# Kernel tuning notes

Hardware: AMD Instinct MI355X
Metric: run time of the kernel (lower is better)

The kernel has to match this reference:

```python
import jax, jax.numpy as jnp
import numpy as np

N_ENT = 2000
GAT_EMB = 64
GAT_HID = 3
HIDDEN = 256
BATCH = 8
ALPHA = 0.2  # LeakyReLU negative slope
MASK_FILL = jnp.float32(9e-15)  # original fills masked-out logits with 9e-15 (NOT -inf)


def setup_inputs() -> dict:
    key = jax.random.key(0)
    k1, k2, k3, k4, k5, k6 = jax.random.split(key, 6)
    emb = jax.random.normal(k1, (N_ENT, GAT_EMB), dtype=jnp.float32)
    W = jax.random.normal(k2, (GAT_EMB, GAT_HID), dtype=jnp.float32) * 0.2
    a = jax.random.normal(k3, (2 * GAT_HID, 1), dtype=jnp.float32) * 0.2
    fc1_w = jax.random.normal(k4, (HIDDEN, N_ENT * GAT_HID), dtype=jnp.float32) * 0.02
    fc1_b = jax.random.normal(k5, (HIDDEN,), dtype=jnp.float32) * 0.02
    adj = jax.random.randint(k6, (BATCH, N_ENT, N_ENT), 0, 2, dtype=jnp.int32)
    return {"emb": emb, "W": W, "a": a, "fc1_w": fc1_w, "fc1_b": fc1_b, "adj": adj}


def reference(emb, W, a, fc1_w, fc1_b, adj):
    # h = emb @ W : [N, 3] -- shared across all graphs in the batch
    h = emb @ W
    # Pairwise logits: original concatenates [h_i, h_j] and dots with a;
    # equivalent to (h @ a1)_i + (h @ a2)_j via broadcasting (no O(N^2*2H) tensor).
    s1 = h @ a[:GAT_HID, 0]   # [N]
    s2 = h @ a[GAT_HID:, 0]   # [N]
    e = jax.nn.leaky_relu(s1[:, None] + s2[None, :], negative_slope=ALPHA)  # [N, N]
    # Mask by adjacency (fill 9e-15, matching original), softmax over neighbors (dim=1)
    masked = jnp.where(adj > 0, e[None, :, :], MASK_FILL)  # [B, N, N]
    att = jax.nn.softmax(masked, axis=2)
    # Weighted aggregation + ELU (concat=True head)
    h_prime = jnp.einsum('bij,jd->bid', att, h)  # [B, N, 3]
    x = jax.nn.elu(h_prime).reshape(att.shape[0], -1)  # [B, N*3]
    return x @ fc1_w.T + fc1_b  # [B, hidden]
```

## Files before the change

kernel.cpp:

```cpp
#include <hip/hip_runtime.h>
#include <cstddef>

#define N_ENT   2000
#define GAT_EMB 64
#define HIDDEN  256
#define BATCH   8
#define ALPHA   0.2f

typedef _Float16 half4 __attribute__((ext_vector_type(4)));

#define WS_HX_OFF      8192
#define WS_HY_OFF      12288
#define WS_HZ_OFF      16384
#define WS_S1_OFF      20480
#define WS_TABLE_BYTES 28672
#define WS_X_OFF       28672
#define WS_TIER2_BYTES 124672

__global__ __launch_bounds__(256) void k_init(const float* __restrict__ fc1_b,
                                              float* __restrict__ out) {
    int idx = blockIdx.x * 256 + threadIdx.x;
    out[idx] = fc1_b[idx & (HIDDEN - 1)];
}

__global__ __launch_bounds__(256) void k_prep(const float* __restrict__ emb,
                                              const float* __restrict__ W,
                                              const float* __restrict__ a,
                                              float* __restrict__ ws) {
    __shared__ float sW[GAT_EMB * 3];
    __shared__ float sa[6];
    int t = threadIdx.x;
    if (t < GAT_EMB * 3) sW[t] = W[t];
    if (t < 6)           sa[t] = a[t];
    __syncthreads();
    int i = blockIdx.x * 256 + t;
    if (i >= N_ENT) return;
    const float4* er = (const float4*)(emb + (size_t)i * GAT_EMB);
    float h0 = 0.f, h1 = 0.f, h2 = 0.f;
#pragma unroll
    for (int k4 = 0; k4 < GAT_EMB / 4; ++k4) {
        float4 e4 = er[k4];
        int k = 4 * k4;
        h0 += e4.x * sW[(k + 0) * 3 + 0]; h1 += e4.x * sW[(k + 0) * 3 + 1]; h2 += e4.x * sW[(k + 0) * 3 + 2];
        h0 += e4.y * sW[(k + 1) * 3 + 0]; h1 += e4.y * sW[(k + 1) * 3 + 1]; h2 += e4.y * sW[(k + 1) * 3 + 2];
        h0 += e4.z * sW[(k + 2) * 3 + 0]; h1 += e4.z * sW[(k + 2) * 3 + 1]; h2 += e4.z * sW[(k + 2) * 3 + 2];
        h0 += e4.w * sW[(k + 3) * 3 + 0]; h1 += e4.w * sW[(k + 3) * 3 + 1]; h2 += e4.w * sW[(k + 3) * 3 + 2];
    }
    ws[i] = h0 * sa[3] + h1 * sa[4] + h2 * sa[5];
    ((_Float16*)((char*)ws + WS_HX_OFF))[i] = (_Float16)h0;
    ((_Float16*)((char*)ws + WS_HY_OFF))[i] = (_Float16)h1;
    ((_Float16*)((char*)ws + WS_HZ_OFF))[i] = (_Float16)h2;
    ws[WS_S1_OFF / 4 + i] = h0 * sa[0] + h1 * sa[1] + h2 * sa[2];
}

__global__ __launch_bounds__(256, 5) void k_main(const float* __restrict__ emb,
                                                 const float* __restrict__ W,
                                                 const float* __restrict__ a,
                                                 const float* __restrict__ fc1_w,
                                                 const int*   __restrict__ adj,
                                                 float* __restrict__ wsf,
                                                 int mode,
                                                 float* __restrict__ out) {
    __shared__ __align__(16) unsigned char smem[20480];
    float*    s2s = (float*)smem;
    _Float16* hxs = (_Float16*)(smem + 8192);
    _Float16* hys = (_Float16*)(smem + 12288);
    _Float16* hzs = (_Float16*)(smem + 16384);
    __shared__ float sW[GAT_EMB * 3];
    __shared__ float sa[6];
    __shared__ float s1sh[16];
    __shared__ float xblk[48];

    int t = threadIdx.x;
    int R0 = blockIdx.x * 16;
    int b  = R0 / N_ENT;
    int i_base = R0 - b * N_ENT;

    if (mode != 0) {
        const uint4* src = (const uint4*)wsf;
        uint4* dst = (uint4*)smem;
#pragma unroll
        for (int rep = 0; rep < 5; ++rep) dst[rep * 256 + t] = src[rep * 256 + t];
        if (t < 16) s1sh[t] = wsf[WS_S1_OFF / 4 + i_base + t];
    } else {
        if (t < GAT_EMB * 3) sW[t] = W[t];
        if (t < 6)           sa[t] = a[t];
        __syncthreads();
        for (int j = t; j < N_ENT; j += 256) {
            const float4* er = (const float4*)(emb + (size_t)j * GAT_EMB);
            float h0 = 0.f, h1 = 0.f, h2 = 0.f;
#pragma unroll
            for (int k4 = 0; k4 < GAT_EMB / 4; ++k4) {
                float4 e4 = er[k4];
                int k = 4 * k4;
                h0 += e4.x * sW[(k + 0) * 3 + 0]; h1 += e4.x * sW[(k + 0) * 3 + 1]; h2 += e4.x * sW[(k + 0) * 3 + 2];
                h0 += e4.y * sW[(k + 1) * 3 + 0]; h1 += e4.y * sW[(k + 1) * 3 + 1]; h2 += e4.y * sW[(k + 1) * 3 + 2];
                h0 += e4.z * sW[(k + 2) * 3 + 0]; h1 += e4.z * sW[(k + 2) * 3 + 1]; h2 += e4.z * sW[(k + 2) * 3 + 2];
                h0 += e4.w * sW[(k + 3) * 3 + 0]; h1 += e4.w * sW[(k + 3) * 3 + 1]; h2 += e4.w * sW[(k + 3) * 3 + 2];
            }
            s2s[j] = h0 * sa[3] + h1 * sa[4] + h2 * sa[5];
            hxs[j] = (_Float16)h0; hys[j] = (_Float16)h1; hzs[j] = (_Float16)h2;
            if (j >= i_base && j < i_base + 16)
                s1sh[j - i_base] = h0 * sa[0] + h1 * sa[1] + h2 * sa[2];
        }
    }
    if (t < 2048 - N_ENT) {
        int j = N_ENT + t;
        s2s[j] = 0.f; hxs[j] = (_Float16)0; hys[j] = (_Float16)0; hzs[j] = (_Float16)0;
    }
    __syncthreads();

    int lane = t & 63;
    int w    = t >> 6;
    float s1r[4];
    const int* __restrict__ rowp[4];
#pragma unroll
    for (int r = 0; r < 4; ++r) {
        s1r[r] = s1sh[4 * w + r];
        rowp[r] = adj + ((size_t)b * N_ENT + (i_base + 4 * w + r)) * N_ENT;
    }

    float acc[4][4];
#pragma unroll
    for (int r = 0; r < 4; ++r) { acc[r][0] = 0.f; acc[r][1] = 0.f; acc[r][2] = 0.f; acc[r][3] = 0.f; }

    int l4 = lane << 2;
#pragma unroll
    for (int c = 0; c < 8; ++c) {
        int j0 = c * 256 + l4;
        bool chunk_full = (c != 7);
        bool valid = chunk_full | (j0 < N_ENT);
        int jc = valid ? j0 : 0;

        int4 m0 = *(const int4*)(rowp[0] + jc);
        int4 m1 = *(const int4*)(rowp[1] + jc);
        int4 m2 = *(const int4*)(rowp[2] + jc);
        int4 m3 = *(const int4*)(rowp[3] + jc);

        float4 s2v = *(const float4*)&s2s[j0];
        half4  hxv = *(const half4*)&hxs[j0];
        half4  hyv = *(const half4*)&hys[j0];
        half4  hzv = *(const half4*)&hzs[j0];
        float hx[4], hy[4], hz[4];
#pragma unroll
        for (int q = 0; q < 4; ++q) { hx[q] = (float)hxv[q]; hy[q] = (float)hyv[q]; hz[q] = (float)hzv[q]; }

        const int* mm[4] = { (const int*)&m0, (const int*)&m1, (const int*)&m2, (const int*)&m3 };
        float vw = valid ? 1.0f : 0.0f;
#pragma unroll
        for (int r = 0; r < 4; ++r) {
#pragma unroll
            for (int q = 0; q < 4; ++q) {
                float e  = s1r[r] + ((const float*)&s2v)[q];
                float ev = __expf(fmaxf(e, 0.f) + ALPHA * fminf(e, 0.f));
                float contrib = (mm[r][q] > 0) ? ev : 1.0f;
                if (!chunk_full) contrib *= vw;
                acc[r][0] += contrib;
                acc[r][1] += contrib * hx[q];
                acc[r][2] += contrib * hy[q];
                acc[r][3] += contrib * hz[q];
            }
        }
    }

#pragma unroll
    for (int off = 32; off > 0; off >>= 1)
#pragma unroll
        for (int r = 0; r < 4; ++r) {
            acc[r][0] += __shfl_xor(acc[r][0], off, 64);
            acc[r][1] += __shfl_xor(acc[r][1], off, 64);
            acc[r][2] += __shfl_xor(acc[r][2], off, 64);
            acc[r][3] += __shfl_xor(acc[r][3], off, 64);
        }

    if (lane == 0) {
#pragma unroll
        for (int r = 0; r < 4; ++r) {
            float inv = 1.f / acc[r][0];
            float p0 = acc[r][1] * inv, p1 = acc[r][2] * inv, p2 = acc[r][3] * inv;
            p0 = (p0 > 0.f) ? p0 : expm1f(p0);
            p1 = (p1 > 0.f) ? p1 : expm1f(p1);
            p2 = (p2 > 0.f) ? p2 : expm1f(p2);
            int c = 3 * (4 * w + r);
            if (mode == 2) {
                _Float16* x16 = (_Float16*)((char*)wsf + WS_X_OFF);
                int i = i_base + 4 * w + r;
                x16[(size_t)(3 * i + 0) * 8 + b] = (_Float16)p0;
                x16[(size_t)(3 * i + 1) * 8 + b] = (_Float16)p1;
                x16[(size_t)(3 * i + 2) * 8 + b] = (_Float16)p2;
            } else {
                xblk[c + 0] = p0; xblk[c + 1] = p1; xblk[c + 2] = p2;
            }
        }
    }

    if (mode != 2) {
        __syncthreads();
        int k = (t + R0) & 255;
        const float* wr = fc1_w + (size_t)k * (N_ENT * 3) + 3 * i_base;
        float d = 0.f;
#pragma unroll
        for (int c4 = 0; c4 < 12; ++c4) {
            float4 wv = *(const float4*)(wr + 4 * c4);
            d += xblk[4 * c4 + 0] * wv.x + xblk[4 * c4 + 1] * wv.y
               + xblk[4 * c4 + 2] * wv.z + xblk[4 * c4 + 3] * wv.w;
        }
        atomicAdd(&out[b * HIDDEN + k], d);
    }
}

__global__ __launch_bounds__(256) void k_fc(const _Float16* __restrict__ x16,
                                            const float* __restrict__ fc1_w,
                                            const float* __restrict__ fc1_b,
                                            float* __restrict__ out) {
    __shared__ float red[4][8];
    int t = threadIdx.x, lane = t & 63, w = t >> 6;
    int k = blockIdx.x;
    const float* __restrict__ wr = fc1_w + (size_t)k * (N_ENT * 3);
    float acc[BATCH];
#pragma unroll
    for (int b = 0; b < BATCH; ++b) acc[b] = 0.f;
#pragma unroll
    for (int it = 0; it < 6; ++it) {
        int m0 = 4 * t + 1024 * it;
        if (m0 + 3 < N_ENT * 3) {
            float4 wv4 = *(const float4*)(wr + m0);
#pragma unroll
            for (int q = 0; q < 4; ++q) {
                half4 xa = *(const half4*)(x16 + (size_t)(m0 + q) * 8);
                half4 xb = *(const half4*)(x16 + (size_t)(m0 + q) * 8 + 4);
                float wv = ((const float*)&wv4)[q];
                acc[0] += wv * (float)xa[0]; acc[1] += wv * (float)xa[1];
                acc[2] += wv * (float)xa[2]; acc[3] += wv * (float)xa[3];
                acc[4] += wv * (float)xb[0]; acc[5] += wv * (float)xb[1];
                acc[6] += wv * (float)xb[2]; acc[7] += wv * (float)xb[3];
            }
        }
    }
#pragma unroll
    for (int off = 32; off > 0; off >>= 1)
#pragma unroll
        for (int b = 0; b < BATCH; ++b) acc[b] += __shfl_xor(acc[b], off, 64);
    if (lane == 0)
#pragma unroll
        for (int b = 0; b < BATCH; ++b) red[w][b] = acc[b];
    __syncthreads();
    if (t < 8)
        out[t * HIDDEN + k] = red[0][t] + red[1][t] + red[2][t] + red[3][t] + fc1_b[k];
}

extern "C" void kernel_launch(void* const* d_in, const int* in_sizes, int n_in,
                              void* d_out, int out_size, void* d_ws, size_t ws_size,
                              hipStream_t stream) {
    const float* emb   = (const float*)d_in[0];
    const float* W     = (const float*)d_in[1];
    const float* a     = (const float*)d_in[2];
    const float* fc1_w = (const float*)d_in[3];
    const float* fc1_b = (const float*)d_in[4];
    const int*   adj   = (const int*)d_in[5];
    float* out = (float*)d_out;
    float* ws  = (float*)d_ws;
    (void)in_sizes; (void)n_in; (void)out_size;

    int tier = (ws_size >= (size_t)WS_TIER2_BYTES) ? 2
             : (ws_size >= (size_t)WS_TABLE_BYTES) ? 1 : 0;

    if (tier < 2)  k_init<<<8, 256, 0, stream>>>(fc1_b, out);
    if (tier >= 1) k_prep<<<8, 256, 0, stream>>>(emb, W, a, ws);
    k_main<<<1000, 256, 0, stream>>>(emb, W, a, fc1_w, adj, ws, tier, out);
    if (tier == 2)
        k_fc<<<HIDDEN, 256, 0, stream>>>((const _Float16*)((char*)d_ws + WS_X_OFF),
                                         fc1_w, fc1_b, out);
}
```

Before: 214.8 us.

## Split attention rows across column slices with a partial-sum buffer and normalize pass

The fused per-row-block kernel is replaced by a k_flat kernel that splits each row's 2000 columns into 8 slices. Each wave processes 16 rows for one slice and writes partial sums (denominator and three weighted sums) to workspace. A new k_norm kernel reduces the slices, applies softmax normalization and ELU, and writes fp16 x for k_fc. This aims to raise parallelism and memory-level concurrency over the 128MB adjacency stream, at the cost of an extra launch, a larger workspace requirement and partial-sum traffic. If the workspace is too small, execution falls back to the old fused kernel.

```diff
diff --git a/kernel.cpp b/kernel.cpp
--- a/kernel.cpp
+++ b/kernel.cpp
@@ -6,6 +6,8 @@
 #define HIDDEN  256
 #define BATCH   8
 #define ALPHA   0.2f
+#define NROWS   (BATCH * N_ENT)
+#define SLICES  8
 
 typedef _Float16 half4 __attribute__((ext_vector_type(4)));
 
@@ -13,9 +15,10 @@
 #define WS_HY_OFF      12288
 #define WS_HZ_OFF      16384
 #define WS_S1_OFF      20480
+#define WS_X_OFF       28672
+#define WS_PART_OFF    124672
 #define WS_TABLE_BYTES 28672
-#define WS_X_OFF       28672
-#define WS_TIER2_BYTES 124672
+#define WS_TIER2_BYTES 2172672
 
 __global__ __launch_bounds__(256) void k_init(const float* __restrict__ fc1_b,
                                               float* __restrict__ out) {
@@ -34,7 +37,15 @@
     if (t < 6)           sa[t] = a[t];
     __syncthreads();
     int i = blockIdx.x * 256 + t;
-    if (i >= N_ENT) return;
+    if (i >= 2048) return;
+    if (i >= N_ENT) {
+        ws[i] = 0.f;
+        ((_Float16*)((char*)ws + WS_HX_OFF))[i] = (_Float16)0;
+        ((_Float16*)((char*)ws + WS_HY_OFF))[i] = (_Float16)0;
+        ((_Float16*)((char*)ws + WS_HZ_OFF))[i] = (_Float16)0;
+        ws[WS_S1_OFF / 4 + i] = 0.f;
+        return;
+    }
     const float4* er = (const float4*)(emb + (size_t)i * GAT_EMB);
     float h0 = 0.f, h1 = 0.f, h2 = 0.f;
 #pragma unroll
@@ -53,14 +64,129 @@
     ws[WS_S1_OFF / 4 + i] = h0 * sa[0] + h1 * sa[1] + h2 * sa[2];
 }
 
-__global__ __launch_bounds__(256, 5) void k_main(const float* __restrict__ emb,
-                                                 const float* __restrict__ W,
-                                                 const float* __restrict__ a,
-                                                 const float* __restrict__ fc1_w,
-                                                 const int*   __restrict__ adj,
-                                                 float* __restrict__ wsf,
-                                                 int mode,
-                                                 float* __restrict__ out) {
+__global__ __launch_bounds__(256) void k_flat(const int* __restrict__ adj,
+                                              const float* __restrict__ wsf,
+                                              float* __restrict__ part) {
+    int t     = threadIdx.x;
+    int lane  = t & 63;
+    int w     = t >> 6;
+    int slice = blockIdx.x & 7;
+    int rgrp  = blockIdx.x >> 3;
+    int r0    = rgrp * 64 + w * 16;
+    int b     = r0 / N_ENT;
+    int i0w   = r0 - b * N_ENT;
+
+    int j0 = slice * 256 + lane * 4;
+    bool valid = (j0 < N_ENT);
+    int jc = valid ? j0 : 0;
+    float vw = valid ? 1.0f : 0.0f;
+
+    float4 s2v = *(const float4*)(wsf + j0);
+    half4  hxv = *(const half4*)((const char*)wsf + WS_HX_OFF + 2 * j0);
+    half4  hyv = *(const half4*)((const char*)wsf + WS_HY_OFF + 2 * j0);
+    half4  hzv = *(const half4*)((const char*)wsf + WS_HZ_OFF + 2 * j0);
+    float s2q[4], hxq[4], hyq[4], hzq[4];
+#pragma unroll
+    for (int q = 0; q < 4; ++q) {
+        s2q[q] = ((const float*)&s2v)[q];
+        hxq[q] = (float)hxv[q]; hyq[q] = (float)hyv[q]; hzq[q] = (float)hzv[q];
+    }
+    const float* __restrict__ s1p = wsf + WS_S1_OFF / 4 + i0w;
+    const int*   __restrict__ rowb = adj + (size_t)r0 * N_ENT;
+    float4* __restrict__ pp = (float4*)part + (size_t)r0 * SLICES + slice;
+
+#pragma unroll 4
+    for (int rr = 0; rr < 16; ++rr) {
+        float s1v = s1p[rr];
+        int4 m = *(const int4*)(rowb + rr * N_ENT + jc);
+        float as = 0.f, ax = 0.f, ay = 0.f, az = 0.f;
+#pragma unroll
+        for (int q = 0; q < 4; ++q) {
+            float e  = s1v + s2q[q];
+            float lr = fmaxf(e, 0.f) + ALPHA * fminf(e, 0.f);
+            float ev = __expf(lr);
+            const int* mi = (const int*)&m;
+            float c = ((mi[q] > 0) ? ev : 1.0f) * vw;
+            as += c; ax += c * hxq[q]; ay += c * hyq[q]; az += c * hzq[q];
+        }
+#pragma unroll
+        for (int off = 32; off > 0; off >>= 1) {
+            as += __shfl_xor(as, off, 64); ax += __shfl_xor(ax, off, 64);
+            ay += __shfl_xor(ay, off, 64); az += __shfl_xor(az, off, 64);
+        }
+        if (lane == 0) pp[(size_t)rr * SLICES] = make_float4(as, ax, ay, az);
+    }
+}
+
+__global__ __launch_bounds__(256) void k_norm(const float* __restrict__ part,
+                                              _Float16* __restrict__ x16) {
+    int row = blockIdx.x * 256 + threadIdx.x;
+    if (row >= NROWS) return;
+    int b = row / N_ENT;
+    int i = row - b * N_ENT;
+    const float4* pp = (const float4*)part + (size_t)row * SLICES;
+    float as = 0.f, ax = 0.f, ay = 0.f, az = 0.f;
+#pragma unroll
+    for (int s = 0; s < SLICES; ++s) {
+        float4 p = pp[s];
+        as += p.x; ax += p.y; ay += p.z; az += p.w;
+    }
+    float inv = 1.f / as;
+    float p0 = ax * inv, p1 = ay * inv, p2 = az * inv;
+    p0 = (p0 > 0.f) ? p0 : expm1f(p0);
+    p1 = (p1 > 0.f) ? p1 : expm1f(p1);
+    p2 = (p2 > 0.f) ? p2 : expm1f(p2);
+    x16[(size_t)(3 * i + 0) * 8 + b] = (_Float16)p0;
+    x16[(size_t)(3 * i + 1) * 8 + b] = (_Float16)p1;
+    x16[(size_t)(3 * i + 2) * 8 + b] = (_Float16)p2;
+}
+
+__global__ __launch_bounds__(256) void k_fc(const _Float16* __restrict__ x16,
+                                            const float* __restrict__ fc1_w,
+                                            const float* __restrict__ fc1_b,
+                                            float* __restrict__ out) {
+    __shared__ float red[4][8];
+    int t = threadIdx.x, lane = t & 63, w = t >> 6;
+    int k = blockIdx.x;
+    const float* __restrict__ wr = fc1_w + (size_t)k * (N_ENT * 3);
+    float acc[BATCH];
+#pragma unroll
+    for (int b = 0; b < BATCH; ++b) acc[b] = 0.f;
+#pragma unroll
+    for (int it = 0; it < 6; ++it) {
+        int m0 = 4 * t + 1024 * it;
+        if (m0 + 3 < N_ENT * 3) {
+            float4 wv4 = *(const float4*)(wr + m0);
+#pragma unroll
+            for (int q = 0; q < 4; ++q) {
+                half4 xa = *(const half4*)(x16 + (size_t)(m0 + q) * 8);
+                half4 xb = *(const half4*)(x16 + (size_t)(m0 + q) * 8 + 4);
+                float wv = ((const float*)&wv4)[q];
+                acc[0] += wv * (float)xa[0]; acc[1] += wv * (float)xa[1];
+                acc[2] += wv * (float)xa[2]; acc[3] += wv * (float)xa[3];
+                acc[4] += wv * (float)xb[0]; acc[5] += wv * (float)xb[1];
+                acc[6] += wv * (float)xb[2]; acc[7] += wv * (float)xb[3];
+            }
+        }
+    }
+#pragma unroll
+    for (int off = 32; off > 0; off >>= 1)
+#pragma unroll
+        for (int b = 0; b < BATCH; ++b) acc[b] += __shfl_xor(acc[b], off, 64);
+    if (lane == 0)
+#pragma unroll
+        for (int b = 0; b < BATCH; ++b) red[w][b] = acc[b];
+    __syncthreads();
+    if (t < 8)
+        out[t * HIDDEN + k] = red[0][t] + red[1][t] + red[2][t] + red[3][t] + fc1_b[k];
+}
+
+__global__ __launch_bounds__(256, 5) void k_main_fb(const float* __restrict__ emb,
+                                                    const float* __restrict__ W,
+                                                    const float* __restrict__ a,
+                                                    const float* __restrict__ fc1_w,
+                                                    const int*   __restrict__ adj,
+                                                    float* __restrict__ out) {
     __shared__ __align__(16) unsigned char smem[20480];
     float*    s2s = (float*)smem;
     _Float16* hxs = (_Float16*)(smem + 8192);
@@ -76,33 +202,25 @@
     int b  = R0 / N_ENT;
     int i_base = R0 - b * N_ENT;
 
-    if (mode != 0) {
-        const uint4* src = (const uint4*)wsf;
-        uint4* dst = (uint4*)smem;
-#pragma unroll
-        for (int rep = 0; rep < 5; ++rep) dst[rep * 256 + t] = src[rep * 256 + t];
-        if (t < 16) s1sh[t] = wsf[WS_S1_OFF / 4 + i_base + t];
-    } else {
-        if (t < GAT_EMB * 3) sW[t] = W[t];
-        if (t < 6)           sa[t] = a[t];
-        __syncthreads();
-        for (int j = t; j < N_ENT; j += 256) {
-            const float4* er = (const float4*)(emb + (size_t)j * GAT_EMB);
-            float h0 = 0.f, h1 = 0.f, h2 = 0.f;
-#pragma unroll
-            for (int k4 = 0; k4 < GAT_EMB / 4; ++k4) {
-                float4 e4 = er[k4];
-                int k = 4 * k4;
-                h0 += e4.x * sW[(k + 0) * 3 + 0]; h1 += e4.x * sW[(k + 0) * 3 + 1]; h2 += e4.x * sW[(k + 0) * 3 + 2];
-                h0 += e4.y * sW[(k + 1) * 3 + 0]; h1 += e4.y * sW[(k + 1) * 3 + 1]; h2 += e4.y * sW[(k + 1) * 3 + 2];
-                h0 += e4.z * sW[(k + 2) * 3 + 0]; h1 += e4.z * sW[(k + 2) * 3 + 1]; h2 += e4.z * sW[(k + 2) * 3 + 2];
-                h0 += e4.w * sW[(k + 3) * 3 + 0]; h1 += e4.w * sW[(k + 3) * 3 + 1]; h2 += e4.w * sW[(k + 3) * 3 + 2];
-            }
-            s2s[j] = h0 * sa[3] + h1 * sa[4] + h2 * sa[5];
-            hxs[j] = (_Float16)h0; hys[j] = (_Float16)h1; hzs[j] = (_Float16)h2;
-            if (j >= i_base && j < i_base + 16)
-                s1sh[j - i_base] = h0 * sa[0] + h1 * sa[1] + h2 * sa[2];
-        }
+    if (t < GAT_EMB * 3) sW[t] = W[t];
+    if (t < 6)           sa[t] = a[t];
+    __syncthreads();
+    for (int j = t; j < N_ENT; j += 256) {
+        const float4* er = (const float4*)(emb + (size_t)j * GAT_EMB);
+        float h0 = 0.f, h1 = 0.f, h2 = 0.f;
+#pragma unroll
+        for (int k4 = 0; k4 < GAT_EMB / 4; ++k4) {
+            float4 e4 = er[k4];
+            int k = 4 * k4;
+            h0 += e4.x * sW[(k + 0) * 3 + 0]; h1 += e4.x * sW[(k + 0) * 3 + 1]; h2 += e4.x * sW[(k + 0) * 3 + 2];
+            h0 += e4.y * sW[(k + 1) * 3 + 0]; h1 += e4.y * sW[(k + 1) * 3 + 1]; h2 += e4.y * sW[(k + 1) * 3 + 2];
+            h0 += e4.z * sW[(k + 2) * 3 + 0]; h1 += e4.z * sW[(k + 2) * 3 + 1]; h2 += e4.z * sW[(k + 2) * 3 + 2];
+            h0 += e4.w * sW[(k + 3) * 3 + 0]; h1 += e4.w * sW[(k + 3) * 3 + 1]; h2 += e4.w * sW[(k + 3) * 3 + 2];
+        }
+        s2s[j] = h0 * sa[3] + h1 * sa[4] + h2 * sa[5];
+        hxs[j] = (_Float16)h0; hys[j] = (_Float16)h1; hzs[j] = (_Float16)h2;
+        if (j >= i_base && j < i_base + 16)
+            s1sh[j - i_base] = h0 * sa[0] + h1 * sa[1] + h2 * sa[2];
     }
     if (t < 2048 - N_ENT) {
         int j = N_ENT + t;
@@ -119,24 +237,19 @@
         s1r[r] = s1sh[4 * w + r];
         rowp[r] = adj + ((size_t)b * N_ENT + (i_base + 4 * w + r)) * N_ENT;
     }
-
     float acc[4][4];
 #pragma unroll
     for (int r = 0; r < 4; ++r) { acc[r][0] = 0.f; acc[r][1] = 0.f; acc[r][2] = 0.f; acc[r][3] = 0.f; }
-
     int l4 = lane << 2;
 #pragma unroll
     for (int c = 0; c < 8; ++c) {
         int j0 = c * 256 + l4;
-        bool chunk_full = (c != 7);
-        bool valid = chunk_full | (j0 < N_ENT);
+        bool valid = (j0 < N_ENT);
         int jc = valid ? j0 : 0;
-
         int4 m0 = *(const int4*)(rowp[0] + jc);
         int4 m1 = *(const int4*)(rowp[1] + jc);
         int4 m2 = *(const int4*)(rowp[2] + jc);
         int4 m3 = *(const int4*)(rowp[3] + jc);
-
         float4 s2v = *(const float4*)&s2s[j0];
         half4  hxv = *(const half4*)&hxs[j0];
         half4  hyv = *(const half4*)&hys[j0];
@@ -144,25 +257,19 @@
         float hx[4], hy[4], hz[4];
 #pragma unroll
         for (int q = 0; q < 4; ++q) { hx[q] = (float)hxv[q]; hy[q] = (float)hyv[q]; hz[q] = (float)hzv[q]; }
-
         const int* mm[4] = { (const int*)&m0, (const int*)&m1, (const int*)&m2, (const int*)&m3 };
         float vw = valid ? 1.0f : 0.0f;
 #pragma unroll
-        for (int r = 0; r < 4; ++r) {
+        for (int r = 0; r < 4; ++r)
 #pragma unroll
             for (int q = 0; q < 4; ++q) {
                 float e  = s1r[r] + ((const float*)&s2v)[q];
                 float ev = __expf(fmaxf(e, 0.f) + ALPHA * fminf(e, 0.f));
-                float contrib = (mm[r][q] > 0) ? ev : 1.0f;
-                if (!chunk_full) contrib *= vw;
-                acc[r][0] += contrib;
-                acc[r][1] += contrib * hx[q];
-                acc[r][2] += contrib * hy[q];
-                acc[r][3] += contrib * hz[q];
+                float contrib = ((mm[r][q] > 0) ? ev : 1.0f) * vw;
+                acc[r][0] += contrib; acc[r][1] += contrib * hx[q];
+                acc[r][2] += contrib * hy[q]; acc[r][3] += contrib * hz[q];
             }
-        }
-    }
-
+    }
 #pragma unroll
     for (int off = 32; off > 0; off >>= 1)
 #pragma unroll
@@ -172,81 +279,27 @@
             acc[r][2] += __shfl_xor(acc[r][2], off, 64);
             acc[r][3] += __shfl_xor(acc[r][3], off, 64);
         }
-
-    if (lane == 0) {
+    if (lane == 0)
 #pragma unroll
         for (int r = 0; r < 4; ++r) {
             float inv = 1.f / acc[r][0];
             float p0 = acc[r][1] * inv, p1 = acc[r][2] * inv, p2 = acc[r][3] * inv;
-            p0 = (p0 > 0.f) ? p0 : expm1f(p0);
-            p1 = (p1 > 0.f) ? p1 : expm1f(p1);
-            p2 = (p2 > 0.f) ? p2 : expm1f(p2);
             int c = 3 * (4 * w + r);
-            if (mode == 2) {
-                _Float16* x16 = (_Float16*)((char*)wsf + WS_X_OFF);
-                int i = i_base + 4 * w + r;
-                x16[(size_t)(3 * i + 0) * 8 + b] = (_Float16)p0;
-                x16[(size_t)(3 * i + 1) * 8 + b] = (_Float16)p1;
-                x16[(size_t)(3 * i + 2) * 8 + b] = (_Float16)p2;
-            } else {
-                xblk[c + 0] = p0; xblk[c + 1] = p1; xblk[c + 2] = p2;
-            }
-        }
-    }
-
-    if (mode != 2) {
-        __syncthreads();
-        int k = (t + R0) & 255;
-        const float* wr = fc1_w + (size_t)k * (N_ENT * 3) + 3 * i_base;
-        float d = 0.f;
-#pragma unroll
-        for (int c4 = 0; c4 < 12; ++c4) {
-            float4 wv = *(const float4*)(wr + 4 * c4);
-            d += xblk[4 * c4 + 0] * wv.x + xblk[4 * c4 + 1] * wv.y
-               + xblk[4 * c4 + 2] * wv.z + xblk[4 * c4 + 3] * wv.w;
-        }
-        atomicAdd(&out[b * HIDDEN + k], d);
-    }
-}
-
-__global__ __launch_bounds__(256) void k_fc(const _Float16* __restrict__ x16,
-                                            const float* __restrict__ fc1_w,
-                                            const float* __restrict__ fc1_b,
-                                            float* __restrict__ out) {
-    __shared__ float red[4][8];
-    int t = threadIdx.x, lane = t & 63, w = t >> 6;
-    int k = blockIdx.x;
-    const float* __restrict__ wr = fc1_w + (size_t)k * (N_ENT * 3);
-    float acc[BATCH];
-#pragma unroll
-    for (int b = 0; b < BATCH; ++b) acc[b] = 0.f;
-#pragma unroll
-    for (int it = 0; it < 6; ++it) {
-        int m0 = 4 * t + 1024 * it;
-        if (m0 + 3 < N_ENT * 3) {
-            float4 wv4 = *(const float4*)(wr + m0);
-#pragma unroll
-            for (int q = 0; q < 4; ++q) {
-                half4 xa = *(const half4*)(x16 + (size_t)(m0 + q) * 8);
-                half4 xb = *(const half4*)(x16 + (size_t)(m0 + q) * 8 + 4);
-                float wv = ((const float*)&wv4)[q];
-                acc[0] += wv * (float)xa[0]; acc[1] += wv * (float)xa[1];
-                acc[2] += wv * (float)xa[2]; acc[3] += wv * (float)xa[3];
-                acc[4] += wv * (float)xb[0]; acc[5] += wv * (float)xb[1];
-                acc[6] += wv * (float)xb[2]; acc[7] += wv * (float)xb[3];
-            }
-        }
-    }
-#pragma unroll
-    for (int off = 32; off > 0; off >>= 1)
-#pragma unroll
-        for (int b = 0; b < BATCH; ++b) acc[b] += __shfl_xor(acc[b], off, 64);
-    if (lane == 0)
-#pragma unroll
-        for (int b = 0; b < BATCH; ++b) red[w][b] = acc[b];
-    __syncthreads();
-    if (t < 8)
-        out[t * HIDDEN + k] = red[0][t] + red[1][t] + red[2][t] + red[3][t] + fc1_b[k];
+            xblk[c + 0] = (p0 > 0.f) ? p0 : expm1f(p0);
+            xblk[c + 1] = (p1 > 0.f) ? p1 : expm1f(p1);
+            xblk[c + 2] = (p2 > 0.f) ? p2 : expm1f(p2);
+        }
+    __syncthreads();
+    int k = (t + R0) & 255;
+    const float* wr = fc1_w + (size_t)k * (N_ENT * 3) + 3 * i_base;
+    float d = 0.f;
+#pragma unroll
+    for (int c4 = 0; c4 < 12; ++c4) {
+        float4 wv = *(const float4*)(wr + 4 * c4);
+        d += xblk[4 * c4 + 0] * wv.x + xblk[4 * c4 + 1] * wv.y
+           + xblk[4 * c4 + 2] * wv.z + xblk[4 * c4 + 3] * wv.w;
+    }
+    atomicAdd(&out[b * HIDDEN + k], d);
 }
 
 extern "C" void kernel_launch(void* const* d_in, const int* in_sizes, int n_in,
@@ -262,13 +315,15 @@
     float* ws  = (float*)d_ws;
     (void)in_sizes; (void)n_in; (void)out_size;
 
-    int tier = (ws_size >= (size_t)WS_TIER2_BYTES) ? 2
-             : (ws_size >= (size_t)WS_TABLE_BYTES) ? 1 : 0;
-
-    if (tier < 2)  k_init<<<8, 256, 0, stream>>>(fc1_b, out);
-    if (tier >= 1) k_prep<<<8, 256, 0, stream>>>(emb, W, a, ws);
-    k_main<<<1000, 256, 0, stream>>>(emb, W, a, fc1_w, adj, ws, tier, out);
-    if (tier == 2)
+    if (ws_size >= (size_t)WS_TIER2_BYTES) {
+        k_prep<<<8, 256, 0, stream>>>(emb, W, a, ws);
+        k_flat<<<2000, 256, 0, stream>>>(adj, ws, ws + WS_PART_OFF / 4);
+        k_norm<<<(NROWS + 255) / 256, 256, 0, stream>>>(ws + WS_PART_OFF / 4,
+                                                        (_Float16*)((char*)d_ws + WS_X_OFF));
         k_fc<<<HIDDEN, 256, 0, stream>>>((const _Float16*)((char*)d_ws + WS_X_OFF),
                                          fc1_w, fc1_b, out);
-}
+    } else {
+        k_init<<<8, 256, 0, stream>>>(fc1_b, out);
+        k_main_fb<<<1000, 256, 0, stream>>>(emb, W, a, fc1_w, adj, out);
+    }
+}
```

After: 219.6 us. 2.2% more time.
